# Optimization experiments

Hardware: AMD Instinct MI355X
Metric: run time of the kernel (lower is better)

The kernel has to match this reference:

```python
import jax, jax.numpy as jnp
import numpy as np

B, N, C, H = 4, 1024, 1024, 16
D = C // H  # head_dim = 64


def _xavier(key, shape, gain):
    fan_in, fan_out = shape[1], shape[0]
    limit = gain * np.sqrt(6.0 / (fan_in + fan_out))
    return jax.random.uniform(key, shape, jnp.float32, -limit, limit)


def setup_inputs() -> dict:
    key = jax.random.key(0)
    ks = jax.random.split(key, 12)
    g = 2.0 ** (-0.5)
    return {
        "x": jax.random.normal(ks[0], (B, N, C), jnp.float32),
        "attn_bias": jax.random.normal(ks[1], (B, H, N, N), jnp.float32),
        "attn_mask": jnp.ones((B, N), jnp.int32),
        "Wq": _xavier(ks[2], (C, C), g), "bq": jnp.zeros((C,), jnp.float32),
        "Wk": _xavier(ks[3], (C, C), g), "bk": jnp.zeros((C,), jnp.float32),
        "Wv": _xavier(ks[4], (C, C), g), "bv": jnp.zeros((C,), jnp.float32),
        "Wo": _xavier(ks[5], (C, C), 1.0), "bo": jnp.zeros((C,), jnp.float32),
    }


def reference(x, attn_bias, attn_mask, Wq, bq, Wk, bk, Wv, bv, Wo, bo):
    scale = D ** (-0.5)
    # projections; nn.Linear computes x @ W.T + b
    def proj(W, b):
        return (x @ W.T + b).reshape(B, N, H, D).transpose(0, 2, 1, 3)  # [B,H,N,D]
    q = proj(Wq, bq) * scale
    k = proj(Wk, bk)
    v = proj(Wv, bv)
    scores = jnp.einsum("bhnd,bhmd->bhnm", q, k)  # [B,H,N,N]
    scores = scores + attn_bias  # attn_bias_type == 'add'
    # 2D mask [B,N] -> [B,1,1,N]; masked_fill where mask == 0
    mask = attn_mask[:, None, None, :]
    scores = jnp.where(mask == 0, -jnp.inf, scores)
    weights = jax.nn.softmax(scores, axis=-1)  # stable (internal max subtract)
    # attn_drop is identity in eval / p=0.0
    out = jnp.einsum("bhnm,bhmd->bhnd", weights, v)
    out = out.transpose(0, 2, 1, 3).reshape(B, N, C)
    return out @ Wo.T + bo
```

## Files before the change

### kernel.cpp

```cpp
#include <hip/hip_runtime.h>
#include <hip/hip_bf16.h>

#define B_ 4
#define N_ 1024
#define C_ 1024
#define H_ 16
#define D_ 64

typedef __attribute__((ext_vector_type(8))) short bf16x8;
typedef __attribute__((ext_vector_type(4))) float f32x4;

__device__ __forceinline__ void gld_lds16(const void* g, void* l) {
    __builtin_amdgcn_global_load_lds(
        (const __attribute__((address_space(1))) void*)g,
        (__attribute__((address_space(3))) void*)l, 16, 0, 0);
}

__global__ __launch_bounds__(256) void f2b_kernel(const float* __restrict__ s,
                                                  __hip_bfloat16* __restrict__ d,
                                                  int n) {
    int i = (blockIdx.x * 256 + threadIdx.x) * 4;
    if (i < n) {
        float4 v = *(const float4*)&s[i];
        d[i + 0] = __float2bfloat16(v.x);
        d[i + 1] = __float2bfloat16(v.y);
        d[i + 2] = __float2bfloat16(v.z);
        d[i + 3] = __float2bfloat16(v.w);
    }
}

__global__ __launch_bounds__(256) void f2b4_kernel(const float* __restrict__ w0,
                                                   const float* __restrict__ w1,
                                                   const float* __restrict__ w2,
                                                   const float* __restrict__ w3,
                                                   __hip_bfloat16* __restrict__ d0,
                                                   __hip_bfloat16* __restrict__ d1,
                                                   __hip_bfloat16* __restrict__ d2,
                                                   __hip_bfloat16* __restrict__ d3) {
    int sel = blockIdx.y;
    const float* s = sel == 0 ? w0 : sel == 1 ? w1 : sel == 2 ? w2 : w3;
    __hip_bfloat16* d = sel == 0 ? d0 : sel == 1 ? d1 : sel == 2 ? d2 : d3;
    int i = (blockIdx.x * 256 + threadIdx.x) * 4;
    float4 v = *(const float4*)&s[i];
    d[i + 0] = __float2bfloat16(v.x);
    d[i + 1] = __float2bfloat16(v.y);
    d[i + 2] = __float2bfloat16(v.z);
    d[i + 3] = __float2bfloat16(v.w);
}

__global__ __launch_bounds__(256) void gemm_qkv(const __hip_bfloat16* __restrict__ A,
                                                const __hip_bfloat16* __restrict__ wq,
                                                const __hip_bfloat16* __restrict__ wk,
                                                const __hip_bfloat16* __restrict__ wv,
                                                const float* __restrict__ bq,
                                                const float* __restrict__ bk,
                                                const float* __restrict__ bv,
                                                __hip_bfloat16* __restrict__ qo,
                                                __hip_bfloat16* __restrict__ ko,
                                                __hip_bfloat16* __restrict__ vto) {
    __shared__ __hip_bfloat16 Al[128 * 32];
    __shared__ __hip_bfloat16 Bl[128 * 32];
    const int sel = blockIdx.x >> 3;
    const __hip_bfloat16* Bw = sel == 0 ? wq : sel == 1 ? wk : wv;
    const float* bias = sel == 0 ? bq : sel == 1 ? bk : bv;
    const int t = threadIdx.x, w = t >> 6, l = t & 63;
    const int wr = w >> 1, wc = w & 1, lr = l & 15, lg = l >> 4;
    const int m0 = blockIdx.y * 128, n0 = (blockIdx.x & 7) * 128;
    const int K = C_;

    f32x4 acc[4][4] = {};

    for (int k0 = 0; k0 < K; k0 += 32) {
#pragma unroll
        for (int it = 0; it < 2; ++it) {
            int i = t + it * 256;
            int r = i >> 2, c8 = (i & 3) * 8;
            gld_lds16(A + (size_t)(m0 + r) * K + k0 + c8, &Al[i * 8]);
            gld_lds16(Bw + (size_t)(n0 + r) * K + k0 + c8, &Bl[i * 8]);
        }
        __syncthreads();
        bf16x8 af[4], bfr[4];
#pragma unroll
        for (int mi = 0; mi < 4; ++mi)
            af[mi] = *(const bf16x8*)&Al[(wr * 64 + mi * 16 + lr) * 32 + lg * 8];
#pragma unroll
        for (int ni = 0; ni < 4; ++ni)
            bfr[ni] = *(const bf16x8*)&Bl[(wc * 64 + ni * 16 + lr) * 32 + lg * 8];
#pragma unroll
        for (int mi = 0; mi < 4; ++mi)
#pragma unroll
            for (int ni = 0; ni < 4; ++ni)
                acc[mi][ni] = __builtin_amdgcn_mfma_f32_16x16x32_bf16(
                    af[mi], bfr[ni], acc[mi][ni], 0, 0, 0);
        __syncthreads();
    }

#pragma unroll
    for (int mi = 0; mi < 4; ++mi) {
#pragma unroll
        for (int ni = 0; ni < 4; ++ni) {
            int col = n0 + wc * 64 + ni * 16 + lr;
            float bb = bias[col];
#pragma unroll
            for (int j = 0; j < 4; ++j) {
                int row = m0 + wr * 64 + mi * 16 + lg * 4 + j;
                float v = acc[mi][ni][j] + bb;
                int bb_ = row >> 10, nn = row & 1023;
                int hh = col >> 6, dd = col & 63;
                if (sel == 0) {
                    qo[(((size_t)bb_ * H_ + hh) * N_ + nn) * D_ + dd] =
                        __float2bfloat16(v * 0.125f);
                } else if (sel == 1) {
                    ko[(((size_t)bb_ * H_ + hh) * N_ + nn) * D_ + dd] =
                        __float2bfloat16(v);
                } else {
                    vto[(((size_t)bb_ * H_ + hh) * D_ + dd) * N_ + nn] =
                        __float2bfloat16(v);
                }
            }
        }
    }
}

__global__ __launch_bounds__(256) void gemm_out(const __hip_bfloat16* __restrict__ A,
                                                const __hip_bfloat16* __restrict__ Bw,
                                                const float* __restrict__ bias,
                                                float* __restrict__ out) {
    __shared__ __hip_bfloat16 Al[128 * 32];
    __shared__ __hip_bfloat16 Bl[128 * 32];
    const int t = threadIdx.x, w = t >> 6, l = t & 63;
    const int wr = w >> 1, wc = w & 1, lr = l & 15, lg = l >> 4;
    const int m0 = blockIdx.y * 128, n0 = blockIdx.x * 128;
    const int K = C_;

    f32x4 acc[4][4] = {};

    for (int k0 = 0; k0 < K; k0 += 32) {
#pragma unroll
        for (int it = 0; it < 2; ++it) {
            int i = t + it * 256;
            int r = i >> 2, c8 = (i & 3) * 8;
            gld_lds16(A + (size_t)(m0 + r) * K + k0 + c8, &Al[i * 8]);
            gld_lds16(Bw + (size_t)(n0 + r) * K + k0 + c8, &Bl[i * 8]);
        }
        __syncthreads();
        bf16x8 af[4], bfr[4];
#pragma unroll
        for (int mi = 0; mi < 4; ++mi)
            af[mi] = *(const bf16x8*)&Al[(wr * 64 + mi * 16 + lr) * 32 + lg * 8];
#pragma unroll
        for (int ni = 0; ni < 4; ++ni)
            bfr[ni] = *(const bf16x8*)&Bl[(wc * 64 + ni * 16 + lr) * 32 + lg * 8];
#pragma unroll
        for (int mi = 0; mi < 4; ++mi)
#pragma unroll
            for (int ni = 0; ni < 4; ++ni)
                acc[mi][ni] = __builtin_amdgcn_mfma_f32_16x16x32_bf16(
                    af[mi], bfr[ni], acc[mi][ni], 0, 0, 0);
        __syncthreads();
    }

#pragma unroll
    for (int mi = 0; mi < 4; ++mi)
#pragma unroll
        for (int ni = 0; ni < 4; ++ni) {
            int col = n0 + wc * 64 + ni * 16 + lr;
            float bb = bias[col];
#pragma unroll
            for (int j = 0; j < 4; ++j) {
                int row = m0 + wr * 64 + mi * 16 + lg * 4 + j;
                out[(size_t)row * C_ + col] = acc[mi][ni][j] + bb;
            }
        }
}

__global__ __launch_bounds__(256) void attn_kernel(const __hip_bfloat16* __restrict__ q,
                                                   const __hip_bfloat16* __restrict__ k,
                                                   const __hip_bfloat16* __restrict__ vt,
                                                   const float* __restrict__ bias,
                                                   const int* __restrict__ mask,
                                                   __hip_bfloat16* __restrict__ ao) {
    const int orig = blockIdx.x;
    const int wg = (orig & 7) * 128 + (orig >> 3);
    const int qt = wg & 15, h = (wg >> 4) & 15, b = wg >> 8;
    const int t = threadIdx.x, w = t >> 6, l = t & 63;
    const int lr = l & 15, lg = l >> 4;

    __shared__ __hip_bfloat16 Kl[2][64 * 64];
    __shared__ __hip_bfloat16 Vl[2][64 * 64];
    __shared__ float Pen[1024];
    __shared__ __hip_bfloat16 Pl[4][16][72];

    const size_t bh = (size_t)b * H_ + h;
    const int qr0 = qt * 64;
    const int myrow = qr0 + w * 16 + lr;
    const int orow_base = qr0 + w * 16 + lg * 4;

    {
        int4 mi = *(const int4*)&mask[b * N_ + t * 4];
        float4 p;
        p.x = mi.x ? 0.f : -1e30f;
        p.y = mi.y ? 0.f : -1e30f;
        p.z = mi.z ? 0.f : -1e30f;
        p.w = mi.w ? 0.f : -1e30f;
        *(float4*)&Pen[t * 4] = p;
    }
    __syncthreads();

    const int c0 = t, c1 = t + 256;
    const int r0 = c0 >> 3, r1 = c1 >> 3;
    const int e0 = ((c0 & 7) * 8) ^ ((r0 & 7) << 3);
    const int e1 = ((c1 & 7) * 8) ^ ((r1 & 7) << 3);
    const __hip_bfloat16* kg0 = k + (bh * N_ + r0) * D_ + e0;
    const __hip_bfloat16* kg1 = k + (bh * N_ + r1) * D_ + e1;
    const __hip_bfloat16* vg0 = vt + (bh * D_ + r0) * N_ + e0;
    const __hip_bfloat16* vg1 = vt + (bh * D_ + r1) * N_ + e1;

    bf16x8 qf[2];
#pragma unroll
    for (int half = 0; half < 2; ++half)
        qf[half] = *(const bf16x8*)&q[(bh * N_ + myrow) * D_ + half * 32 + lg * 8];

    const float* brow = bias + ((size_t)bh * N_ + myrow) * N_;
    const int swz = (lr & 7) << 3;

    f32x4 acc[4] = {};
    float m_ = -3e38f, l_ = 0.f;

    __builtin_amdgcn_sched_barrier(0);
    gld_lds16(kg0, &Kl[0][(w * 64) * 8]);
    gld_lds16(kg1, &Kl[0][(256 + w * 64) * 8]);
    gld_lds16(vg0, &Vl[0][(w * 64) * 8]);
    gld_lds16(vg1, &Vl[0][(256 + w * 64) * 8]);
    f32x4 bcur[4];
#pragma unroll
    for (int nkb = 0; nkb < 4; ++nkb)
        bcur[nkb] = *(const f32x4*)&brow[nkb * 16 + lg * 4];
    __builtin_amdgcn_sched_barrier(0);

#pragma unroll
    for (int kt = 0; kt < 16; ++kt) {
        const int ktn = kt < 15 ? kt + 1 : 15;

        gld_lds16(kg0 + (size_t)ktn * 4096, &Kl[(kt + 1) & 1][(w * 64) * 8]);
        gld_lds16(kg1 + (size_t)ktn * 4096, &Kl[(kt + 1) & 1][(256 + w * 64) * 8]);
        gld_lds16(vg0 + ktn * 64, &Vl[(kt + 1) & 1][(w * 64) * 8]);
        gld_lds16(vg1 + ktn * 64, &Vl[(kt + 1) & 1][(256 + w * 64) * 8]);
        f32x4 bnxt[4];
#pragma unroll
        for (int nkb = 0; nkb < 4; ++nkb)
            bnxt[nkb] = *(const f32x4*)&brow[ktn * 64 + nkb * 16 + lg * 4];
        __builtin_amdgcn_sched_barrier(0);
        asm volatile("s_waitcnt vmcnt(8)" ::: "memory");
        __builtin_amdgcn_sched_barrier(0);
        __builtin_amdgcn_s_barrier();
        __builtin_amdgcn_sched_barrier(0);

        const __hip_bfloat16* Kb = &Kl[kt & 1][0];
        float s[4][4];
#pragma unroll
        for (int nkb = 0; nkb < 4; ++nkb) {
            f32x4 a = {};
#pragma unroll
            for (int half = 0; half < 2; ++half) {
                bf16x8 kf = *(const bf16x8*)
                    &Kb[(nkb * 16 + lr) * 64 + ((half * 32 + lg * 8) ^ swz)];
                a = __builtin_amdgcn_mfma_f32_16x16x32_bf16(kf, qf[half], a, 0, 0, 0);
            }
            f32x4 pen = *(const f32x4*)&Pen[kt * 64 + nkb * 16 + lg * 4];
#pragma unroll
            for (int j = 0; j < 4; ++j) s[nkb][j] = a[j] + bcur[nkb][j] + pen[j];
        }

        float tm = s[0][0];
#pragma unroll
        for (int nkb = 0; nkb < 4; ++nkb)
#pragma unroll
            for (int j = 0; j < 4; ++j) tm = fmaxf(tm, s[nkb][j]);
        tm = fmaxf(tm, __shfl_xor(tm, 16));
        tm = fmaxf(tm, __shfl_xor(tm, 32));
        const float mn = fmaxf(m_, tm);
        const float al = __expf(m_ - mn);
        m_ = mn;
        float ts = 0.f;
#pragma unroll
        for (int nkb = 0; nkb < 4; ++nkb)
#pragma unroll
            for (int j = 0; j < 4; ++j) {
                float p = __expf(s[nkb][j] - mn);
                s[nkb][j] = p;
                ts += p;
            }
        ts += __shfl_xor(ts, 16);
        ts += __shfl_xor(ts, 32);
        l_ = l_ * al + ts;

#pragma unroll
        for (int nkb = 0; nkb < 4; ++nkb) {
            __hip_bfloat16 pk[4];
#pragma unroll
            for (int j = 0; j < 4; ++j) pk[j] = __float2bfloat16(s[nkb][j]);
            *(short4*)&Pl[w][lr][nkb * 16 + lg * 4] = *(const short4*)pk;
        }

        float alr[4];
#pragma unroll
        for (int j = 0; j < 4; ++j) alr[j] = __shfl(al, lg * 4 + j);
#pragma unroll
        for (int db = 0; db < 4; ++db)
#pragma unroll
            for (int j = 0; j < 4; ++j) acc[db][j] *= alr[j];

        const __hip_bfloat16* Vb = &Vl[kt & 1][0];
        bf16x8 paf[2];
        paf[0] = *(const bf16x8*)&Pl[w][lr][lg * 8];
        paf[1] = *(const bf16x8*)&Pl[w][lr][32 + lg * 8];
#pragma unroll
        for (int db = 0; db < 4; ++db)
#pragma unroll
            for (int mh = 0; mh < 2; ++mh) {
                bf16x8 vf = *(const bf16x8*)
                    &Vb[(db * 16 + lr) * 64 + ((mh * 32 + lg * 8) ^ swz)];
                acc[db] = __builtin_amdgcn_mfma_f32_16x16x32_bf16(paf[mh], vf,
                                                                  acc[db], 0, 0, 0);
            }

#pragma unroll
        for (int nkb = 0; nkb < 4; ++nkb) bcur[nkb] = bnxt[nkb];

        __builtin_amdgcn_sched_barrier(0);
        __builtin_amdgcn_s_barrier();
        __builtin_amdgcn_sched_barrier(0);
    }

    float dummy = 0.f;
#pragma unroll
    for (int nkb = 0; nkb < 4; ++nkb) dummy += bcur[nkb][0];
    asm volatile("" :: "v"(dummy));

    float linv[4];
#pragma unroll
    for (int j = 0; j < 4; ++j) linv[j] = 1.f / __shfl(l_, lg * 4 + j);
#pragma unroll
    for (int db = 0; db < 4; ++db)
#pragma unroll
        for (int j = 0; j < 4; ++j)
            ao[((size_t)b * N_ + orow_base + j) * C_ + h * 64 + db * 16 + lr] =
                __float2bfloat16(acc[db][j] * linv[j]);
}

extern "C" void kernel_launch(void* const* d_in, const int* in_sizes, int n_in,
                              void* d_out, int out_size, void* d_ws, size_t ws_size,
                              hipStream_t stream) {
    const float* x    = (const float*)d_in[0];
    const float* bias = (const float*)d_in[1];
    const int*   mask = (const int*)d_in[2];
    const float* Wq   = (const float*)d_in[3];
    const float* bq   = (const float*)d_in[4];
    const float* Wk   = (const float*)d_in[5];
    const float* bk   = (const float*)d_in[6];
    const float* Wv   = (const float*)d_in[7];
    const float* bv   = (const float*)d_in[8];
    const float* Wo   = (const float*)d_in[9];
    const float* bo   = (const float*)d_in[10];
    float* out = (float*)d_out;

    char* ws = (char*)d_ws;
    const size_t MB = 1u << 20;
    __hip_bfloat16* xb  = (__hip_bfloat16*)(ws + 0 * MB);
    __hip_bfloat16* wqb = (__hip_bfloat16*)(ws + 8 * MB);
    __hip_bfloat16* wkb = (__hip_bfloat16*)(ws + 10 * MB);
    __hip_bfloat16* wvb = (__hip_bfloat16*)(ws + 12 * MB);
    __hip_bfloat16* wob = (__hip_bfloat16*)(ws + 14 * MB);
    __hip_bfloat16* qb  = (__hip_bfloat16*)(ws + 16 * MB);
    __hip_bfloat16* kb  = (__hip_bfloat16*)(ws + 24 * MB);
    __hip_bfloat16* vtb = (__hip_bfloat16*)(ws + 32 * MB);
    __hip_bfloat16* aob = (__hip_bfloat16*)(ws + 40 * MB);

    f2b_kernel<<<4096, 256, 0, stream>>>(x, xb, B_ * N_ * C_);
    f2b4_kernel<<<dim3(1024, 4), 256, 0, stream>>>(Wq, Wk, Wv, Wo, wqb, wkb, wvb, wob);

    gemm_qkv<<<dim3(24, 32), 256, 0, stream>>>(xb, wqb, wkb, wvb, bq, bk, bv, qb, kb, vtb);

    attn_kernel<<<B_ * H_ * (N_ / 64), 256, 0, stream>>>(qb, kb, vtb, bias, mask, aob);

    gemm_out<<<dim3(8, 32), 256, 0, stream>>>(aob, wob, bo, out);
}
```

Measured before the change: 171.3 us.

## Widen GEMM K-tile with swizzled LDS and double attention block size

Both projection GEMMs now load 64-wide K tiles into XOR-swizzled LDS and run two MFMA sub-steps per barrier pair, so they synchronise half as often and avoid LDS bank conflicts. The attention kernel moves to 512 threads covering 128 query rows per block. Each K/V tile in LDS is therefore shared by twice as many queries, and each thread issues fewer loads. It also raises wave priority around the MFMA sections with s_setprio. The risks are higher LDS and register pressure, lower occupancy, and an s_waitcnt count that must match the new number of loads.

```diff
diff --git a/kernel.cpp b/kernel.cpp
--- a/kernel.cpp
+++ b/kernel.cpp
@@ -58,8 +58,8 @@
                                                 __hip_bfloat16* __restrict__ qo,
                                                 __hip_bfloat16* __restrict__ ko,
                                                 __hip_bfloat16* __restrict__ vto) {
-    __shared__ __hip_bfloat16 Al[128 * 32];
-    __shared__ __hip_bfloat16 Bl[128 * 32];
+    __shared__ __hip_bfloat16 Al[128 * 64];
+    __shared__ __hip_bfloat16 Bl[128 * 64];
     const int sel = blockIdx.x >> 3;
     const __hip_bfloat16* Bw = sel == 0 ? wq : sel == 1 ? wk : wv;
     const float* bias = sel == 0 ? bq : sel == 1 ? bk : bv;
@@ -67,31 +67,38 @@
     const int wr = w >> 1, wc = w & 1, lr = l & 15, lg = l >> 4;
     const int m0 = blockIdx.y * 128, n0 = (blockIdx.x & 7) * 128;
     const int K = C_;
+    const int swz = (lr & 7) << 3;
 
     f32x4 acc[4][4] = {};
 
-    for (int k0 = 0; k0 < K; k0 += 32) {
-#pragma unroll
-        for (int it = 0; it < 2; ++it) {
-            int i = t + it * 256;
-            int r = i >> 2, c8 = (i & 3) * 8;
-            gld_lds16(A + (size_t)(m0 + r) * K + k0 + c8, &Al[i * 8]);
-            gld_lds16(Bw + (size_t)(n0 + r) * K + k0 + c8, &Bl[i * 8]);
+    for (int k0 = 0; k0 < K; k0 += 64) {
+#pragma unroll
+        for (int it = 0; it < 4; ++it) {
+            int c = t + it * 256;
+            int r = c >> 3;
+            int e = ((c & 7) * 8) ^ ((r & 7) << 3);
+            gld_lds16(A + (size_t)(m0 + r) * K + k0 + e, &Al[c * 8]);
+            gld_lds16(Bw + (size_t)(n0 + r) * K + k0 + e, &Bl[c * 8]);
         }
         __syncthreads();
-        bf16x8 af[4], bfr[4];
-#pragma unroll
-        for (int mi = 0; mi < 4; ++mi)
-            af[mi] = *(const bf16x8*)&Al[(wr * 64 + mi * 16 + lr) * 32 + lg * 8];
-#pragma unroll
-        for (int ni = 0; ni < 4; ++ni)
-            bfr[ni] = *(const bf16x8*)&Bl[(wc * 64 + ni * 16 + lr) * 32 + lg * 8];
-#pragma unroll
-        for (int mi = 0; mi < 4; ++mi)
+#pragma unroll
+        for (int kk = 0; kk < 2; ++kk) {
+            bf16x8 af[4], bfr[4];
+#pragma unroll
+            for (int mi = 0; mi < 4; ++mi)
+                af[mi] = *(const bf16x8*)
+                    &Al[(wr * 64 + mi * 16 + lr) * 64 + ((kk * 32 + lg * 8) ^ swz)];
 #pragma unroll
             for (int ni = 0; ni < 4; ++ni)
-                acc[mi][ni] = __builtin_amdgcn_mfma_f32_16x16x32_bf16(
-                    af[mi], bfr[ni], acc[mi][ni], 0, 0, 0);
+                bfr[ni] = *(const bf16x8*)
+                    &Bl[(wc * 64 + ni * 16 + lr) * 64 + ((kk * 32 + lg * 8) ^ swz)];
+#pragma unroll
+            for (int mi = 0; mi < 4; ++mi)
+#pragma unroll
+                for (int ni = 0; ni < 4; ++ni)
+                    acc[mi][ni] = __builtin_amdgcn_mfma_f32_16x16x32_bf16(
+                        af[mi], bfr[ni], acc[mi][ni], 0, 0, 0);
+        }
         __syncthreads();
     }
 
@@ -126,37 +133,44 @@
                                                 const __hip_bfloat16* __restrict__ Bw,
                                                 const float* __restrict__ bias,
                                                 float* __restrict__ out) {
-    __shared__ __hip_bfloat16 Al[128 * 32];
-    __shared__ __hip_bfloat16 Bl[128 * 32];
+    __shared__ __hip_bfloat16 Al[128 * 64];
+    __shared__ __hip_bfloat16 Bl[128 * 64];
     const int t = threadIdx.x, w = t >> 6, l = t & 63;
     const int wr = w >> 1, wc = w & 1, lr = l & 15, lg = l >> 4;
     const int m0 = blockIdx.y * 128, n0 = blockIdx.x * 128;
     const int K = C_;
+    const int swz = (lr & 7) << 3;
 
     f32x4 acc[4][4] = {};
 
-    for (int k0 = 0; k0 < K; k0 += 32) {
-#pragma unroll
-        for (int it = 0; it < 2; ++it) {
-            int i = t + it * 256;
-            int r = i >> 2, c8 = (i & 3) * 8;
-            gld_lds16(A + (size_t)(m0 + r) * K + k0 + c8, &Al[i * 8]);
-            gld_lds16(Bw + (size_t)(n0 + r) * K + k0 + c8, &Bl[i * 8]);
+    for (int k0 = 0; k0 < K; k0 += 64) {
+#pragma unroll
+        for (int it = 0; it < 4; ++it) {
+            int c = t + it * 256;
+            int r = c >> 3;
+            int e = ((c & 7) * 8) ^ ((r & 7) << 3);
+            gld_lds16(A + (size_t)(m0 + r) * K + k0 + e, &Al[c * 8]);
+            gld_lds16(Bw + (size_t)(n0 + r) * K + k0 + e, &Bl[c * 8]);
         }
         __syncthreads();
-        bf16x8 af[4], bfr[4];
-#pragma unroll
-        for (int mi = 0; mi < 4; ++mi)
-            af[mi] = *(const bf16x8*)&Al[(wr * 64 + mi * 16 + lr) * 32 + lg * 8];
-#pragma unroll
-        for (int ni = 0; ni < 4; ++ni)
-            bfr[ni] = *(const bf16x8*)&Bl[(wc * 64 + ni * 16 + lr) * 32 + lg * 8];
-#pragma unroll
-        for (int mi = 0; mi < 4; ++mi)
+#pragma unroll
+        for (int kk = 0; kk < 2; ++kk) {
+            bf16x8 af[4], bfr[4];
+#pragma unroll
+            for (int mi = 0; mi < 4; ++mi)
+                af[mi] = *(const bf16x8*)
+                    &Al[(wr * 64 + mi * 16 + lr) * 64 + ((kk * 32 + lg * 8) ^ swz)];
 #pragma unroll
             for (int ni = 0; ni < 4; ++ni)
-                acc[mi][ni] = __builtin_amdgcn_mfma_f32_16x16x32_bf16(
-                    af[mi], bfr[ni], acc[mi][ni], 0, 0, 0);
+                bfr[ni] = *(const bf16x8*)
+                    &Bl[(wc * 64 + ni * 16 + lr) * 64 + ((kk * 32 + lg * 8) ^ swz)];
+#pragma unroll
+            for (int mi = 0; mi < 4; ++mi)
+#pragma unroll
+                for (int ni = 0; ni < 4; ++ni)
+                    acc[mi][ni] = __builtin_amdgcn_mfma_f32_16x16x32_bf16(
+                        af[mi], bfr[ni], acc[mi][ni], 0, 0, 0);
+        }
         __syncthreads();
     }
 
@@ -174,47 +188,41 @@
         }
 }
 
-__global__ __launch_bounds__(256) void attn_kernel(const __hip_bfloat16* __restrict__ q,
-                                                   const __hip_bfloat16* __restrict__ k,
-                                                   const __hip_bfloat16* __restrict__ vt,
-                                                   const float* __restrict__ bias,
-                                                   const int* __restrict__ mask,
-                                                   __hip_bfloat16* __restrict__ ao) {
+__global__ __launch_bounds__(512, 4) void attn_kernel(const __hip_bfloat16* __restrict__ q,
+                                                      const __hip_bfloat16* __restrict__ k,
+                                                      const __hip_bfloat16* __restrict__ vt,
+                                                      const float* __restrict__ bias,
+                                                      const int* __restrict__ mask,
+                                                      __hip_bfloat16* __restrict__ ao) {
     const int orig = blockIdx.x;
-    const int wg = (orig & 7) * 128 + (orig >> 3);
-    const int qt = wg & 15, h = (wg >> 4) & 15, b = wg >> 8;
+    const int wg = (orig & 7) * 64 + (orig >> 3);
+    const int qt = wg & 7, h = (wg >> 3) & 15, b = wg >> 7;
     const int t = threadIdx.x, w = t >> 6, l = t & 63;
     const int lr = l & 15, lg = l >> 4;
 
     __shared__ __hip_bfloat16 Kl[2][64 * 64];
     __shared__ __hip_bfloat16 Vl[2][64 * 64];
     __shared__ float Pen[1024];
-    __shared__ __hip_bfloat16 Pl[4][16][72];
+    __shared__ __hip_bfloat16 Pl[8][16][72];
 
     const size_t bh = (size_t)b * H_ + h;
-    const int qr0 = qt * 64;
+    const int qr0 = qt * 128;
     const int myrow = qr0 + w * 16 + lr;
     const int orow_base = qr0 + w * 16 + lg * 4;
 
     {
-        int4 mi = *(const int4*)&mask[b * N_ + t * 4];
-        float4 p;
+        int2 mi = *(const int2*)&mask[b * N_ + t * 2];
+        float2 p;
         p.x = mi.x ? 0.f : -1e30f;
         p.y = mi.y ? 0.f : -1e30f;
-        p.z = mi.z ? 0.f : -1e30f;
-        p.w = mi.w ? 0.f : -1e30f;
-        *(float4*)&Pen[t * 4] = p;
+        *(float2*)&Pen[t * 2] = p;
     }
     __syncthreads();
 
-    const int c0 = t, c1 = t + 256;
-    const int r0 = c0 >> 3, r1 = c1 >> 3;
-    const int e0 = ((c0 & 7) * 8) ^ ((r0 & 7) << 3);
-    const int e1 = ((c1 & 7) * 8) ^ ((r1 & 7) << 3);
+    const int r0 = t >> 3;
+    const int e0 = ((t & 7) * 8) ^ ((r0 & 7) << 3);
     const __hip_bfloat16* kg0 = k + (bh * N_ + r0) * D_ + e0;
-    const __hip_bfloat16* kg1 = k + (bh * N_ + r1) * D_ + e1;
     const __hip_bfloat16* vg0 = vt + (bh * D_ + r0) * N_ + e0;
-    const __hip_bfloat16* vg1 = vt + (bh * D_ + r1) * N_ + e1;
 
     bf16x8 qf[2];
 #pragma unroll
@@ -229,9 +237,7 @@
 
     __builtin_amdgcn_sched_barrier(0);
     gld_lds16(kg0, &Kl[0][(w * 64) * 8]);
-    gld_lds16(kg1, &Kl[0][(256 + w * 64) * 8]);
     gld_lds16(vg0, &Vl[0][(w * 64) * 8]);
-    gld_lds16(vg1, &Vl[0][(256 + w * 64) * 8]);
     f32x4 bcur[4];
 #pragma unroll
     for (int nkb = 0; nkb < 4; ++nkb)
@@ -243,21 +249,20 @@
         const int ktn = kt < 15 ? kt + 1 : 15;
 
         gld_lds16(kg0 + (size_t)ktn * 4096, &Kl[(kt + 1) & 1][(w * 64) * 8]);
-        gld_lds16(kg1 + (size_t)ktn * 4096, &Kl[(kt + 1) & 1][(256 + w * 64) * 8]);
         gld_lds16(vg0 + ktn * 64, &Vl[(kt + 1) & 1][(w * 64) * 8]);
-        gld_lds16(vg1 + ktn * 64, &Vl[(kt + 1) & 1][(256 + w * 64) * 8]);
         f32x4 bnxt[4];
 #pragma unroll
         for (int nkb = 0; nkb < 4; ++nkb)
             bnxt[nkb] = *(const f32x4*)&brow[ktn * 64 + nkb * 16 + lg * 4];
         __builtin_amdgcn_sched_barrier(0);
-        asm volatile("s_waitcnt vmcnt(8)" ::: "memory");
+        asm volatile("s_waitcnt vmcnt(6)" ::: "memory");
         __builtin_amdgcn_sched_barrier(0);
         __builtin_amdgcn_s_barrier();
         __builtin_amdgcn_sched_barrier(0);
 
         const __hip_bfloat16* Kb = &Kl[kt & 1][0];
         float s[4][4];
+        __builtin_amdgcn_s_setprio(1);
 #pragma unroll
         for (int nkb = 0; nkb < 4; ++nkb) {
             f32x4 a = {};
@@ -271,6 +276,7 @@
 #pragma unroll
             for (int j = 0; j < 4; ++j) s[nkb][j] = a[j] + bcur[nkb][j] + pen[j];
         }
+        __builtin_amdgcn_s_setprio(0);
 
         float tm = s[0][0];
 #pragma unroll
@@ -315,6 +321,7 @@
         bf16x8 paf[2];
         paf[0] = *(const bf16x8*)&Pl[w][lr][lg * 8];
         paf[1] = *(const bf16x8*)&Pl[w][lr][32 + lg * 8];
+        __builtin_amdgcn_s_setprio(1);
 #pragma unroll
         for (int db = 0; db < 4; ++db)
 #pragma unroll
@@ -324,6 +331,7 @@
                 acc[db] = __builtin_amdgcn_mfma_f32_16x16x32_bf16(paf[mh], vf,
                                                                   acc[db], 0, 0, 0);
             }
+        __builtin_amdgcn_s_setprio(0);
 
 #pragma unroll
         for (int nkb = 0; nkb < 4; ++nkb) bcur[nkb] = bnxt[nkb];
@@ -382,7 +390,7 @@
 
     gemm_qkv<<<dim3(24, 32), 256, 0, stream>>>(xb, wqb, wkb, wvb, bq, bk, bv, qb, kb, vtb);
 
-    attn_kernel<<<B_ * H_ * (N_ / 64), 256, 0, stream>>>(qb, kb, vtb, bias, mask, aob);
+    attn_kernel<<<B_ * H_ * (N_ / 128), 512, 0, stream>>>(qb, kb, vtb, bias, mask, aob);
 
     gemm_out<<<dim3(8, 32), 256, 0, stream>>>(aob, wob, bo, out);
 }
```

Result: no change. 173.9 us (+1.5%).
